# Optimization experiments

Hardware: AMD Instinct MI355X
Metric: run time of the kernel (lower is better)

Reference implementation:

```python
import jax, jax.numpy as jnp
import numpy as np
from jax import lax

B, C, L, K = 8, 256, 4096, 65
PAD = K // 2  # torch: int(kernel.shape[-1] / 2) = 32 -> same-length output for odd K


def depthwise_corr(x, k):
    """Depthwise cross-correlation (torch conv1d semantics, no kernel flip).
    x: [B, C, L] float32, k: [K] float32 (same kernel shared by all channels,
    matching kernel.repeat(seq_len, 1)). Returns [B, C, L]."""
    w = jnp.broadcast_to(k.reshape(1, 1, K), (C, 1, K))  # [C, 1, K]
    return lax.conv_general_dilated(
        x, w, window_strides=(1,), padding=[(PAD, PAD)],
        dimension_numbers=("NCH", "OIH", "NCH"), feature_group_count=C)


def setup_inputs() -> dict:
    key = jax.random.key(0)
    k1, k2, k3 = jax.random.split(key, 3)
    return {
        "x": jax.random.normal(k1, (B, C, L), dtype=jnp.float32),
        "kernel_real": jax.random.normal(k2, (K,), dtype=jnp.float32),
        "kernel_imag": jax.random.normal(k3, (K,), dtype=jnp.float32),
        "weights_mag": jnp.ones((1, C, 1), dtype=jnp.float32),
        "weights_angle": jnp.ones((1, C, 1), dtype=jnp.float32),
    }


def reference(x, kernel_real, kernel_imag, weights_mag, weights_angle):
    # mf_coeffs = conj(kernel) -> weight = kernel_real - 1j*kernel_imag.
    # Input x is real (imag=0 after .to(complex64)), so complex conv splits
    # into two real depthwise correlations.
    yr = depthwise_corr(x, kernel_real)            # [B, C, L]
    yi = -depthwise_corr(x, kernel_imag)           # [B, C, L]
    y = lax.complex(yr, yi)                        # complex64 [B, C, L]

    # torch.std over dims (1,2), unbiased (correction=1), complex -> real std
    mean = jnp.mean(y, axis=(1, 2), keepdims=True)
    n = C * L
    var = jnp.sum(jnp.abs(y - mean) ** 2, axis=(1, 2), keepdims=True) / (n - 1)
    y = y / jnp.sqrt(var)                          # real std broadcasts over complex

    # weights_mag * y * exp(-1j * weights_angle)
    phase = lax.complex(jnp.cos(weights_angle), -jnp.sin(weights_angle))  # [1, C, 1]
    y = weights_mag * y * phase

    # FFT over the channel dim (dim=-2), then fftshift on that dim
    return jnp.fft.fftshift(jnp.fft.fft(y, axis=-2), axes=-2)
```

## Files before the change

### kernel.cpp

```cpp
#include <hip/hip_runtime.h>
#include <math.h>

#define NB 8
#define NC 256
#define NL 4096
#define NK 65
#define NSL (NL / 16)

typedef float vf4 __attribute__((ext_vector_type(4)));
typedef float vf2 __attribute__((ext_vector_type(2)));

__device__ float4 g_part[NB * NSL];

__device__ __forceinline__ int lidx(int row, int q) {
    return (row << 3) + (q ^ (row & 7));
}

#define PKFMA_EVEN(ACC, WP, K2)                                             \
    asm("v_pk_fma_f32 %0, %1, %2, %0 op_sel:[0,0,0] op_sel_hi:[0,1,1]"      \
        : "+v"(ACC) : "v"(WP), "v"(K2))
#define PKFMA_ODD(ACC, WP, K2)                                              \
    asm("v_pk_fma_f32 %0, %1, %2, %0 op_sel:[1,0,0] op_sel_hi:[1,1,1]"      \
        : "+v"(ACC) : "v"(WP), "v"(K2))

#define LOAD16P(W2, off)                                                    \
    {                                                                       \
        const int g0_ = l0 + (off);                                         \
        if (g0_ >= 0 && g0_ + 16 <= NL) {         \
            _Pragma("unroll")                                               \
            for (int q = 0; q < 4; ++q) {                                   \
                const float4 v_ = *(const float4*)(xr + g0_ + 4 * q);       \
                vf2 a_; a_.x = v_.x; a_.y = v_.y; W2[2*q]   = a_;           \
                vf2 b_; b_.x = v_.z; b_.y = v_.w; W2[2*q+1] = b_;           \
            }                                                               \
        } else {                                                            \
            _Pragma("unroll")                                               \
            for (int q = 0; q < 8; ++q) {                                   \
                const int g_ = g0_ + 2 * q;                                 \
                vf2 a_;                                                     \
                a_.x = (g_     >= 0 && g_     < NL) ? xr[g_]     : 0.0f;    \
                a_.y = (g_ + 1 >= 0 && g_ + 1 < NL) ? xr[g_ + 1] : 0.0f;    \
                W2[q] = a_;                                                 \
            }                                                               \
        }                                                                   \
    }

#define CHUNK16PK(LoP, HiP, tb)                                             \
    {                                                                       \
        _Pragma("unroll")                                                   \
        for (int j2 = 0; j2 < 16; ++j2) {                                   \
            vf2 k2_; k2_.x = kre[(tb) + j2]; k2_.y = kim[(tb) + j2];        \
            _Pragma("unroll")                                               \
            for (int i = 0; i < 16; ++i) {                                  \
                const int w_ = i + j2;                                      \
                const int p_ = w_ >> 1;                                     \
                vf2 wp_ = (p_ < 8) ? LoP[p_] : HiP[p_ - 8];                 \
                if ((w_ & 1) == 0) { PKFMA_EVEN(s2[i], wp_, k2_); }         \
                else               { PKFMA_ODD (s2[i], wp_, k2_); }         \
            }                                                               \
        }                                                                   \
    }

__device__ __forceinline__ int digitrev_shift(int pp) {
    int k = ((pp & 3) << 6) | (((pp >> 2) & 3) << 4)
          | (((pp >> 4) & 3) << 2) | ((pp >> 6) & 3);
    return k ^ 128;
}

__global__ __launch_bounds__(256, 4) void fused_conv_fft_kernel(
    const float* __restrict__ x,
    const float* __restrict__ kre,
    const float* __restrict__ kim,
    const float* __restrict__ wmag,
    const float* __restrict__ wang,
    float* __restrict__ out,
    int out_size)
{
    __shared__ __align__(16) float4 lbuf4[NC * 8];

    const int t = threadIdx.x;
    const int b = blockIdx.x & 7;
    const int st = blockIdx.x >> 3;
    const int l0 = st << 4;
    const int lane = t & 63, wv = t >> 6;

    const float* xr = x + (size_t)b * NC * NL + (size_t)t * NL;
    const bool interleaved = (out_size >= 2 * NB * NC * NL);

    vf2 s2[16];
    #pragma unroll
    for (int i = 0; i < 16; ++i) { s2[i].x = 0.0f; s2[i].y = 0.0f; }

    vf2 W0[8], W1[8], W2[8], W3[8];
    LOAD16P(W0, -32);
    LOAD16P(W1, -16);
    LOAD16P(W2, 0);
    LOAD16P(W3, 16);
    CHUNK16PK(W0, W1, 0);
    LOAD16P(W0, 32);
    CHUNK16PK(W1, W2, 16);
    CHUNK16PK(W2, W3, 32);
    CHUNK16PK(W3, W0, 48);
    {
        vf2 k2_; k2_.x = kre[64]; k2_.y = kim[64];
        #pragma unroll
        for (int i = 0; i < 16; ++i) {
            vf2 wp_ = W0[i >> 1];
            if ((i & 1) == 0) { PKFMA_EVEN(s2[i], wp_, k2_); }
            else              { PKFMA_ODD (s2[i], wp_, k2_); }
        }
    }

    vf2 tsum; tsum.x = 0.0f; tsum.y = 0.0f;
    vf2 tsq2; tsq2.x = 0.0f; tsq2.y = 0.0f;
    #pragma unroll
    for (int i = 0; i < 16; ++i) {
        tsum = tsum + s2[i];
        tsq2 = __builtin_elementwise_fma(s2[i], s2[i], tsq2);
    }
    float tsr = tsum.x, tsi = -tsum.y, tsq = tsq2.x + tsq2.y;

    float sw, cw;
    sincosf(wang[t], &sw, &cw);
    const float wm = wmag[t];
    const float wgr =  wm * cw;
    const float wgi = -wm * sw;
    float tw64r, tw64i;
    {
        float ang = (float)lane * 0.024543692606170260f;
        float s, c;
        sincosf(ang, &s, &c);
        tw64r = c; tw64i = -s;
    }

    #pragma unroll
    for (int k = 0; k < 8; ++k) {
        float srA = s2[2*k].x,   siA = s2[2*k].y;
        float srB = s2[2*k+1].x, siB = s2[2*k+1].y;
        float4 o;
        o.x = srA * wgr + siA * wgi;
        o.y = srA * wgi - siA * wgr;
        o.z = srB * wgr + siB * wgi;
        o.w = srB * wgi - siB * wgr;
        lbuf4[lidx(t, k)] = o;
    }
    __syncthreads();

    #pragma unroll
    for (int s = 0; s < 3; ++s) {
        const int shift = 2 * s;
        const int q = 64 >> shift;
        #pragma unroll
        for (int it = 0; it < 2; ++it) {
            int task = it * 256 + t;
            int lpp = task & 7;
            int m = task >> 3;
            int j = m & (q - 1);
            int blk = m >> (6 - shift);
            int base2 = blk << (8 - shift);

            int ca = base2 + j;
            float4 a0 = lbuf4[lidx(ca, lpp)];
            float4 a1 = lbuf4[lidx(ca + q, lpp)];
            float4 a2 = lbuf4[lidx(ca + 2*q, lpp)];
            float4 a3 = lbuf4[lidx(ca + 3*q, lpp)];

            int e = j << shift;
            float w1r = __shfl(tw64r, e);
            float w1i = __shfl(tw64i, e);
            float w2r = fmaf(w1r, w1r, -(w1i * w1i));
            float w2i = 2.0f * w1r * w1i;
            float w3r = w2r * w1r - w2i * w1i;
            float w3i = w2r * w1i + w2i * w1r;

            float4 b0, b1, b2, b3;
            {
                float t0r = a0.x + a2.x, t0i = a0.y + a2.y;
                float t1r = a0.x - a2.x, t1i = a0.y - a2.y;
                float t2r = a1.x + a3.x, t2i = a1.y + a3.y;
                float t3r = a1.x - a3.x, t3i = a1.y - a3.y;
                b0.x = t0r + t2r;       b0.y = t0i + t2i;
                float b2r = t0r - t2r,  b2i = t0i - t2i;
                float b1r = t1r + t3i,  b1i = t1i - t3r;
                float b3r = t1r - t3i,  b3i = t1i + t3r;
                b1.x = b1r*w1r - b1i*w1i;  b1.y = b1r*w1i + b1i*w1r;
                b2.x = b2r*w2r - b2i*w2i;  b2.y = b2r*w2i + b2i*w2r;
                b3.x = b3r*w3r - b3i*w3i;  b3.y = b3r*w3i + b3i*w3r;
            }
            {
                float t0r = a0.z + a2.z, t0i = a0.w + a2.w;
                float t1r = a0.z - a2.z, t1i = a0.w - a2.w;
                float t2r = a1.z + a3.z, t2i = a1.w + a3.w;
                float t3r = a1.z - a3.z, t3i = a1.w - a3.w;
                b0.z = t0r + t2r;       b0.w = t0i + t2i;
                float b2r = t0r - t2r,  b2i = t0i - t2i;
                float b1r = t1r + t3i,  b1i = t1i - t3r;
                float b3r = t1r - t3i,  b3i = t1i + t3r;
                b1.z = b1r*w1r - b1i*w1i;  b1.w = b1r*w1i + b1i*w1r;
                b2.z = b2r*w2r - b2i*w2i;  b2.w = b2r*w2i + b2i*w2r;
                b3.z = b3r*w3r - b3i*w3i;  b3.w = b3r*w3i + b3i*w3r;
            }
            lbuf4[lidx(ca, lpp)]         = b0;
            lbuf4[lidx(ca + q, lpp)]     = b1;
            lbuf4[lidx(ca + 2*q, lpp)]   = b2;
            lbuf4[lidx(ca + 3*q, lpp)]   = b3;
        }
        __syncthreads();
    }

    #pragma unroll
    for (int it = 0; it < 2; ++it) {
        int task = it * 256 + t;
        int lpp = task & 7;
        int m = task >> 3;
        int ca = m << 2;
        float4 a0 = lbuf4[lidx(ca + 0, lpp)];
        float4 a1 = lbuf4[lidx(ca + 1, lpp)];
        float4 a2 = lbuf4[lidx(ca + 2, lpp)];
        float4 a3 = lbuf4[lidx(ca + 3, lpp)];

        float4 b0, b1, b2, b3;
        {
            float t0r = a0.x + a2.x, t0i = a0.y + a2.y;
            float t1r = a0.x - a2.x, t1i = a0.y - a2.y;
            float t2r = a1.x + a3.x, t2i = a1.y + a3.y;
            float t3r = a1.x - a3.x, t3i = a1.y - a3.y;
            b0.x = t0r + t2r;  b0.y = t0i + t2i;
            b2.x = t0r - t2r;  b2.y = t0i - t2i;
            b1.x = t1r + t3i;  b1.y = t1i - t3r;
            b3.x = t1r - t3i;  b3.y = t1i + t3r;
        }
        {
            float t0r = a0.z + a2.z, t0i = a0.w + a2.w;
            float t1r = a0.z - a2.z, t1i = a0.w - a2.w;
            float t2r = a1.z + a3.z, t2i = a1.w + a3.w;
            float t3r = a1.z - a3.z, t3i = a1.w - a3.w;
            b0.z = t0r + t2r;  b0.w = t0i + t2i;
            b2.z = t0r - t2r;  b2.w = t0i - t2i;
            b1.z = t1r + t3i;  b1.w = t1i - t3r;
            b3.z = t1r - t3i;  b3.w = t1i + t3r;
        }

        float4 bb[4] = { b0, b1, b2, b3 };
        #pragma unroll
        for (int mm = 0; mm < 4; ++mm) {
            int cout = digitrev_shift(ca + mm);
            float4 v = bb[mm];
            if (interleaved) {
                size_t fi = 2 * ((size_t)(b * NC + cout) * NL + l0) + 4 * lpp;
                if (fi + 4 <= (size_t)out_size) {
                    *(float4*)(out + fi) = v;
                }
            } else {
                size_t fi = (size_t)(b * NC + cout) * NL + l0 + 2 * lpp;
                if (fi + 2 <= (size_t)out_size) {
                    float2 o2; o2.x = v.x; o2.y = v.z;
                    *(float2*)(out + fi) = o2;
                }
            }
        }
    }

    #pragma unroll
    for (int off = 32; off > 0; off >>= 1) {
        tsr += __shfl_down(tsr, off);
        tsi += __shfl_down(tsi, off);
        tsq += __shfl_down(tsq, off);
    }
    __syncthreads();
    float* redf = (float*)lbuf4;
    if (lane == 0) { redf[wv*3+0] = tsr; redf[wv*3+1] = tsi; redf[wv*3+2] = tsq; }
    __syncthreads();
    if (t == 0) {
        float a0 = 0.0f, a1 = 0.0f, a2 = 0.0f;
        #pragma unroll
        for (int i = 0; i < 4; ++i) { a0 += redf[i*3]; a1 += redf[i*3+1]; a2 += redf[i*3+2]; }
        g_part[b * NSL + st] = make_float4(a0, a1, a2, 0.0f);
    }
}

__global__ __launch_bounds__(256) void scale_out_kernel(
    float* __restrict__ out, int out_size)
{
    __shared__ float sred[13];
    const int t = threadIdx.x;
    const int j = blockIdx.x;
    const int b = j & 7;
    const int seg = j >> 3;
    const int lane = t & 63, wv = t >> 6;

    float4 p = g_part[b * NSL + t];
    float psr = p.x, psi = p.y, psq = p.z;
    #pragma unroll
    for (int off = 32; off > 0; off >>= 1) {
        psr += __shfl_down(psr, off);
        psi += __shfl_down(psi, off);
        psq += __shfl_down(psq, off);
    }
    if (lane == 0) { sred[wv*3+0] = psr; sred[wv*3+1] = psi; sred[wv*3+2] = psq; }
    __syncthreads();
    if (t == 0) {
        float a0 = 0.0f, a1 = 0.0f, a2 = 0.0f;
        #pragma unroll
        for (int i = 0; i < 4; ++i) { a0 += sred[i*3]; a1 += sred[i*3+1]; a2 += sred[i*3+2]; }
        const float n = (float)(NC * NL);
        float var = (a2 - (a0*a0 + a1*a1)/n) / (n - 1.0f);
        sred[12] = rsqrtf(var);
    }
    __syncthreads();
    const float inv = sred[12];

    const int fpbatch = out_size >> 3;
    const int fpseg = fpbatch >> 8;
    const int base = b * fpbatch + seg * fpseg;
    if ((fpseg & 3) == 0 && ((size_t)(out + base) & 15) == 0) {
        float4* o4 = (float4*)(out + base);
        const int n4 = fpseg >> 2;
        for (int i = t; i < n4; i += 256) {
            float4 v = o4[i];
            v.x *= inv; v.y *= inv; v.z *= inv; v.w *= inv;
            o4[i] = v;
        }
    } else {
        for (int i = t; i < fpseg; i += 256) out[base + i] *= inv;
    }
    if (j == 2047) {
        for (int i = ((out_size >> 11) << 11) + t; i < out_size; i += 256)
            out[i] *= inv;
    }
}

extern "C" void kernel_launch(void* const* d_in, const int* in_sizes, int n_in,
                              void* d_out, int out_size, void* d_ws, size_t ws_size,
                              hipStream_t stream)
{
    const float* x   = (const float*)d_in[0];
    const float* kre = (const float*)d_in[1];
    const float* kim = (const float*)d_in[2];
    const float* wm  = (const float*)d_in[3];
    const float* wa  = (const float*)d_in[4];
    float* out = (float*)d_out;
    (void)d_ws; (void)ws_size;

    fused_conv_fft_kernel<<<NB * NSL, 256, 0, stream>>>(x, kre, kim, wm, wa,
                                                        out, out_size);
    scale_out_kernel<<<2048, 256, 0, stream>>>(out, out_size);
}
```

Baseline: 139.3 us.

## Restructure channel FFT as register-resident 16x16 decomposition with two LDS passes

Replaces the four-stage radix-4 FFT across channels, which did an LDS round trip and a barrier per stage, with a 16x16 four-step decomposition. Each thread now holds 16 complex values in registers and runs two radix-4 stages locally, so only two LDS exchanges and fewer barriers are needed. The LDS layout changes from float4 pairs to float2 with a new XOR swizzle meant to avoid bank conflicts. In exchange, register pressure rises (32 extra floats per thread), which could reduce occupancy under the 4-blocks launch bound. Global stores shrink from float4 to float2 per thread, which may reduce coalescing.

```diff
diff --git a/kernel.cpp b/kernel.cpp
--- a/kernel.cpp
+++ b/kernel.cpp
@@ -12,8 +12,8 @@
 
 __device__ float4 g_part[NB * NSL];
 
-__device__ __forceinline__ int lidx(int row, int q) {
-    return (row << 3) + (q ^ (row & 7));
+__device__ __forceinline__ int sidx(int row, int p) {
+    return (row << 4) + (p ^ (row & 15) ^ ((row >> 4) & 15));
 }
 
 #define PKFMA_EVEN(ACC, WP, K2)                                             \
@@ -67,6 +67,21 @@
     return k ^ 128;
 }
 
+#define BFLY(A0, A1, A2, A3, W1R, W1I, W2R, W2I, W3R, W3I)                  \
+    {                                                                       \
+        float t0r = A0.x + A2.x, t0i = A0.y + A2.y;                         \
+        float t1r = A0.x - A2.x, t1i = A0.y - A2.y;                         \
+        float t2r = A1.x + A3.x, t2i = A1.y + A3.y;                         \
+        float t3r = A1.x - A3.x, t3i = A1.y - A3.y;                         \
+        A0.x = t0r + t2r;       A0.y = t0i + t2i;                           \
+        float b2r = t0r - t2r,  b2i = t0i - t2i;                            \
+        float b1r = t1r + t3i,  b1i = t1i - t3r;                            \
+        float b3r = t1r - t3i,  b3i = t1i + t3r;                            \
+        A1.x = b1r*(W1R) - b1i*(W1I);  A1.y = b1r*(W1I) + b1i*(W1R);        \
+        A2.x = b2r*(W2R) - b2i*(W2I);  A2.y = b2r*(W2I) + b2i*(W2R);        \
+        A3.x = b3r*(W3R) - b3i*(W3I);  A3.y = b3r*(W3I) + b3i*(W3R);        \
+    }
+
 __global__ __launch_bounds__(256, 4) void fused_conv_fft_kernel(
     const float* __restrict__ x,
     const float* __restrict__ kre,
@@ -76,7 +91,7 @@
     float* __restrict__ out,
     int out_size)
 {
-    __shared__ __align__(16) float4 lbuf4[NC * 8];
+    __shared__ __align__(16) float2 lb2[NC * 16];
 
     const int t = threadIdx.x;
     const int b = blockIdx.x & 7;
@@ -134,128 +149,86 @@
     }
 
     #pragma unroll
-    for (int k = 0; k < 8; ++k) {
-        float srA = s2[2*k].x,   siA = s2[2*k].y;
-        float srB = s2[2*k+1].x, siB = s2[2*k+1].y;
-        float4 o;
+    for (int p = 0; p < 16; ++p) {
+        float srA = s2[p].x, siA = s2[p].y;
+        float2 o;
         o.x = srA * wgr + siA * wgi;
         o.y = srA * wgi - siA * wgr;
-        o.z = srB * wgr + siB * wgi;
-        o.w = srB * wgi - siB * wgr;
-        lbuf4[lidx(t, k)] = o;
-    }
-    __syncthreads();
-
-    #pragma unroll
-    for (int s = 0; s < 3; ++s) {
-        const int shift = 2 * s;
-        const int q = 64 >> shift;
-        #pragma unroll
-        for (int it = 0; it < 2; ++it) {
-            int task = it * 256 + t;
-            int lpp = task & 7;
-            int m = task >> 3;
-            int j = m & (q - 1);
-            int blk = m >> (6 - shift);
-            int base2 = blk << (8 - shift);
-
-            int ca = base2 + j;
-            float4 a0 = lbuf4[lidx(ca, lpp)];
-            float4 a1 = lbuf4[lidx(ca + q, lpp)];
-            float4 a2 = lbuf4[lidx(ca + 2*q, lpp)];
-            float4 a3 = lbuf4[lidx(ca + 3*q, lpp)];
-
-            int e = j << shift;
+        lb2[sidx(t, p)] = o;
+    }
+    __syncthreads();
+
+    {
+        const int j = t & 15, pos = t >> 4;
+        float2 z[16];
+        #pragma unroll
+        for (int k = 0; k < 16; ++k) z[k] = lb2[sidx(j + 16*k, pos)];
+
+        #pragma unroll
+        for (int i = 0; i < 4; ++i) {
+            int e = j + 16*i;
             float w1r = __shfl(tw64r, e);
             float w1i = __shfl(tw64i, e);
-            float w2r = fmaf(w1r, w1r, -(w1i * w1i));
+            float w2r = fmaf(w1r, w1r, -(w1i*w1i));
             float w2i = 2.0f * w1r * w1i;
-            float w3r = w2r * w1r - w2i * w1i;
-            float w3i = w2r * w1i + w2i * w1r;
-
-            float4 b0, b1, b2, b3;
-            {
-                float t0r = a0.x + a2.x, t0i = a0.y + a2.y;
-                float t1r = a0.x - a2.x, t1i = a0.y - a2.y;
-                float t2r = a1.x + a3.x, t2i = a1.y + a3.y;
-                float t3r = a1.x - a3.x, t3i = a1.y - a3.y;
-                b0.x = t0r + t2r;       b0.y = t0i + t2i;
-                float b2r = t0r - t2r,  b2i = t0i - t2i;
-                float b1r = t1r + t3i,  b1i = t1i - t3r;
-                float b3r = t1r - t3i,  b3i = t1i + t3r;
-                b1.x = b1r*w1r - b1i*w1i;  b1.y = b1r*w1i + b1i*w1r;
-                b2.x = b2r*w2r - b2i*w2i;  b2.y = b2r*w2i + b2i*w2r;
-                b3.x = b3r*w3r - b3i*w3i;  b3.y = b3r*w3i + b3i*w3r;
+            float w3r = w2r*w1r - w2i*w1i;
+            float w3i = w2r*w1i + w2i*w1r;
+            BFLY(z[i], z[i+4], z[i+8], z[i+12], w1r,w1i, w2r,w2i, w3r,w3i);
+        }
+        {
+            int e = 4*j;
+            float w1r = __shfl(tw64r, e);
+            float w1i = __shfl(tw64i, e);
+            float w2r = fmaf(w1r, w1r, -(w1i*w1i));
+            float w2i = 2.0f * w1r * w1i;
+            float w3r = w2r*w1r - w2i*w1i;
+            float w3i = w2r*w1i + w2i*w1r;
+            #pragma unroll
+            for (int blk = 0; blk < 4; ++blk) {
+                BFLY(z[4*blk], z[4*blk+1], z[4*blk+2], z[4*blk+3],
+                     w1r,w1i, w2r,w2i, w3r,w3i);
             }
-            {
-                float t0r = a0.z + a2.z, t0i = a0.w + a2.w;
-                float t1r = a0.z - a2.z, t1i = a0.w - a2.w;
-                float t2r = a1.z + a3.z, t2i = a1.w + a3.w;
-                float t3r = a1.z - a3.z, t3i = a1.w - a3.w;
-                b0.z = t0r + t2r;       b0.w = t0i + t2i;
-                float b2r = t0r - t2r,  b2i = t0i - t2i;
-                float b1r = t1r + t3i,  b1i = t1i - t3r;
-                float b3r = t1r - t3i,  b3i = t1i + t3r;
-                b1.z = b1r*w1r - b1i*w1i;  b1.w = b1r*w1i + b1i*w1r;
-                b2.z = b2r*w2r - b2i*w2i;  b2.w = b2r*w2i + b2i*w2r;
-                b3.z = b3r*w3r - b3i*w3i;  b3.w = b3r*w3i + b3i*w3r;
-            }
-            lbuf4[lidx(ca, lpp)]         = b0;
-            lbuf4[lidx(ca + q, lpp)]     = b1;
-            lbuf4[lidx(ca + 2*q, lpp)]   = b2;
-            lbuf4[lidx(ca + 3*q, lpp)]   = b3;
-        }
-        __syncthreads();
-    }
-
-    #pragma unroll
-    for (int it = 0; it < 2; ++it) {
-        int task = it * 256 + t;
-        int lpp = task & 7;
-        int m = task >> 3;
-        int ca = m << 2;
-        float4 a0 = lbuf4[lidx(ca + 0, lpp)];
-        float4 a1 = lbuf4[lidx(ca + 1, lpp)];
-        float4 a2 = lbuf4[lidx(ca + 2, lpp)];
-        float4 a3 = lbuf4[lidx(ca + 3, lpp)];
-
-        float4 b0, b1, b2, b3;
-        {
-            float t0r = a0.x + a2.x, t0i = a0.y + a2.y;
-            float t1r = a0.x - a2.x, t1i = a0.y - a2.y;
-            float t2r = a1.x + a3.x, t2i = a1.y + a3.y;
-            float t3r = a1.x - a3.x, t3i = a1.y - a3.y;
-            b0.x = t0r + t2r;  b0.y = t0i + t2i;
-            b2.x = t0r - t2r;  b2.y = t0i - t2i;
-            b1.x = t1r + t3i;  b1.y = t1i - t3r;
-            b3.x = t1r - t3i;  b3.y = t1i + t3r;
-        }
-        {
-            float t0r = a0.z + a2.z, t0i = a0.w + a2.w;
-            float t1r = a0.z - a2.z, t1i = a0.w - a2.w;
-            float t2r = a1.z + a3.z, t2i = a1.w + a3.w;
-            float t3r = a1.z - a3.z, t3i = a1.w - a3.w;
-            b0.z = t0r + t2r;  b0.w = t0i + t2i;
-            b2.z = t0r - t2r;  b2.w = t0i - t2i;
-            b1.z = t1r + t3i;  b1.w = t1i - t3r;
-            b3.z = t1r - t3i;  b3.w = t1i + t3r;
-        }
-
-        float4 bb[4] = { b0, b1, b2, b3 };
-        #pragma unroll
-        for (int mm = 0; mm < 4; ++mm) {
-            int cout = digitrev_shift(ca + mm);
-            float4 v = bb[mm];
+        }
+        #pragma unroll
+        for (int k = 0; k < 16; ++k) lb2[sidx(j + 16*k, pos)] = z[k];
+    }
+    __syncthreads();
+
+    {
+        const int R = t & 15, pos = t >> 4;
+        float2 y[16];
+        #pragma unroll
+        for (int s = 0; s < 16; ++s) y[s] = lb2[sidx(16*R + s, pos)];
+
+        const float c16r  =  0.92387953251128674f, c16i  = -0.38268343236508978f;
+        const float c32r  =  0.70710678118654757f, c32i  = -0.70710678118654746f;
+        const float c48r  =  0.38268343236508984f, c48i  = -0.92387953251128674f;
+        const float c64r  =  0.0f,                 c64i  = -1.0f;
+        const float c96r  = -0.70710678118654746f, c96i  = -0.70710678118654757f;
+        const float c144r = -0.92387953251128674f, c144i =  0.38268343236508984f;
+        BFLY(y[0], y[4], y[8],  y[12], 1.0f,0.0f, 1.0f,0.0f, 1.0f,0.0f);
+        BFLY(y[1], y[5], y[9],  y[13], c16r,c16i, c32r,c32i, c48r,c48i);
+        BFLY(y[2], y[6], y[10], y[14], c32r,c32i, c64r,c64i, c96r,c96i);
+        BFLY(y[3], y[7], y[11], y[15], c48r,c48i, c96r,c96i, c144r,c144i);
+        #pragma unroll
+        for (int d = 0; d < 4; ++d) {
+            BFLY(y[4*d], y[4*d+1], y[4*d+2], y[4*d+3],
+                 1.0f,0.0f, 1.0f,0.0f, 1.0f,0.0f);
+        }
+
+        #pragma unroll
+        for (int s = 0; s < 16; ++s) {
+            int pp = 16*R + s;
+            int cout = digitrev_shift(pp);
             if (interleaved) {
-                size_t fi = 2 * ((size_t)(b * NC + cout) * NL + l0) + 4 * lpp;
-                if (fi + 4 <= (size_t)out_size) {
-                    *(float4*)(out + fi) = v;
+                size_t fi = 2 * ((size_t)(b * NC + cout) * NL + l0 + pos);
+                if (fi + 2 <= (size_t)out_size) {
+                    *(float2*)(out + fi) = y[s];
                 }
             } else {
-                size_t fi = (size_t)(b * NC + cout) * NL + l0 + 2 * lpp;
-                if (fi + 2 <= (size_t)out_size) {
-                    float2 o2; o2.x = v.x; o2.y = v.z;
-                    *(float2*)(out + fi) = o2;
+                size_t fi = (size_t)(b * NC + cout) * NL + l0 + pos;
+                if (fi < (size_t)out_size) {
+                    out[fi] = y[s].x;
                 }
             }
         }
@@ -268,7 +241,7 @@
         tsq += __shfl_down(tsq, off);
     }
     __syncthreads();
-    float* redf = (float*)lbuf4;
+    float* redf = (float*)lb2;
     if (lane == 0) { redf[wv*3+0] = tsr; redf[wv*3+1] = tsi; redf[wv*3+2] = tsq; }
     __syncthreads();
     if (t == 0) {
```

Result: slower. 155.5 us (+11.6%).
